# Kernel tuning notes

Measured on AMD Instinct MI355X. Metric: run time of the kernel, lower is better.

## Reference

```python
import jax, jax.numpy as jnp
import numpy as np

N_TOKENS = 8192
D_MODEL = 2048
TOP_K = 2
N_S1 = N_TOKENS * TOP_K  # expanded (token, expert-slot) rows after top-k routing
N_S2 = 8192              # rows re-gathered for the second (intra-node) stage


def setup_inputs() -> dict:
    key = jax.random.key(0)
    k_x, k_i1, k_i2 = jax.random.split(key, 3)
    x = jax.random.normal(k_x, (N_TOKENS, D_MODEL), dtype=jnp.float32)
    # Expanded indices sorted by expert bin (upstream radix-sort of bin_ids).
    indices_s1 = jnp.sort(jax.random.randint(k_i1, (N_S1,), 0, N_S1, dtype=jnp.int64))
    # Map from s1-expert layout rows into the s2 stage layout.
    s1exp_to_s2_indices = jax.random.randint(k_i2, (N_S2,), 0, N_S1, dtype=jnp.int64)
    return {
        "x": x,
        "indices_s1": indices_s1,
        "s1exp_to_s2_indices": s1exp_to_s2_indices,
        "n_tokens": N_TOKENS,
        "top_k": TOP_K,
    }


def reference(x, indices_s1, s1exp_to_s2_indices, n_tokens, top_k):
    # Stage 1: gather_with_token_drop -- expanded index // top_k recovers the
    # source token row; rows are already ordered by expert bin (bins encode
    # capacity/drops, reflected in the length of indices_s1).
    dx_s1 = jnp.take(x, indices_s1 // top_k, axis=0)          # [N_S1, d]
    # _AllToAllSingle(ep_group): pure data exchange; on a single shard the
    # split-and-exchange with ins_s1/outs_s1 is the identity permutation.
    dx_s1_exp = dx_s1
    # Stage 2: s1_to_s2_gather -- re-gather rows into the intra-node layout
    # ordered by (bin_ids_s2, bins_s2).
    dx_s2 = jnp.take(dx_s1_exp, s1exp_to_s2_indices, axis=0)  # [N_S2, d]
    # _AllToAllSingle(local_group): identity on a single shard.
    dx_s2_exp = dx_s2
    # Final local ordering: s2 (intra-node) rows first, then s1 (global) rows.
    return jnp.concatenate([dx_s2_exp, dx_s1_exp], axis=0)    # [N_S2 + N_S1, d]
```

## Files before the change

kernel.cpp:

```cpp
#include <hip/hip_runtime.h>
#include <hip/hip_bf16.h>


typedef float v4f __attribute__((ext_vector_type(4)));

__global__ __launch_bounds__(256) void rb_dispatch_kernel(
    const float* __restrict__ x,
    const int* __restrict__ idx_s1,
    const int* __restrict__ idx_s2,
    const int* __restrict__ top_k_ptr,
    float* __restrict__ out,
    int n_s2, int n_rows, int nvec ) {
  const int wave = threadIdx.x >> 6;
  const int lane = threadIdx.x & 63;
  const int row = blockIdx.x * 4 + wave;
  if (row >= n_rows) return;

  const int top_k = *top_k_ptr;

  int src;
  if (row < n_s2) {
    src = idx_s1[idx_s2[row]] / top_k;
  } else {
    src = idx_s1[row - n_s2] / top_k;
  }

  const int d = nvec * 4;
  const v4f* __restrict__ sp = (const v4f*)(x + (size_t)src * (size_t)d);
  v4f* __restrict__ dp = (v4f*)(out + (size_t)row * (size_t)d);

  #pragma unroll 4
  for (int i = lane; i < nvec; i += 64) {
    v4f v = sp[i];
    __builtin_nontemporal_store(v, dp + i);
  }
}

extern "C" void kernel_launch(void* const* d_in, const int* in_sizes, int n_in,
                              void* d_out, int out_size, void* d_ws, size_t ws_size,
                              hipStream_t stream) {
  const float* x      = (const float*)d_in[0];
  const int*   idx_s1 = (const int*)d_in[1];
  const int*   idx_s2 = (const int*)d_in[2];
  const int*   top_k  = (const int*)d_in[4];
  float*       out    = (float*)d_out;

  const int n_s1   = in_sizes[1];
  const int n_s2   = in_sizes[2];
  const int n_rows = n_s1 + n_s2;
  const int d      = out_size / n_rows;
  const int nvec   = d / 4;

  const int rows_per_block = 4;
  const int grid = (n_rows + rows_per_block - 1) / rows_per_block;

  rb_dispatch_kernel<<<grid, 256, 0, stream>>>(
      x, idx_s1, idx_s2, top_k, out, n_s2, n_rows, nvec);
}
```

Measured before the change: 255.7 us.

## Process two rows per wave with XCD-aware block remap and duplicate-source reuse

Each wave now copies two consecutive output rows instead of one, and the block count is halved. Block indices are remapped so that consecutive logical blocks are spread across the 8 XCDs. For d=2048 the kernel uses a fully unrolled 8-vector register copy, and when both rows share a source token it reuses the loaded registers instead of reading x again. Because the s1 indices are sorted and two slots map to one token, adjacent rows often share a source, which could save reads. The remap assumes n_blocks is divisible by 8; otherwise some blocks would be skipped or duplicated.

```diff
diff --git a/kernel.cpp b/kernel.cpp
--- a/kernel.cpp
+++ b/kernel.cpp
@@ -10,29 +10,57 @@
     const int* __restrict__ idx_s2,
     const int* __restrict__ top_k_ptr,
     float* __restrict__ out,
-    int n_s2, int n_rows, int nvec ) {
+    int n_s2, int n_rows, int n_blocks, int nvec ) {
+  const int b = blockIdx.x;
+  const int v = (b & 7) * (n_blocks >> 3) + (b >> 3);
+
   const int wave = threadIdx.x >> 6;
   const int lane = threadIdx.x & 63;
-  const int row = blockIdx.x * 4 + wave;
-  if (row >= n_rows) return;
+  const int r0 = v * 8 + wave * 2;
+  const int r1 = r0 + 1;
+  if (r0 >= n_rows) return;
 
   const int top_k = *top_k_ptr;
 
-  int src;
-  if (row < n_s2) {
-    src = idx_s1[idx_s2[row]] / top_k;
+  int s0, s1;
+  if (r0 < n_s2) s0 = idx_s1[idx_s2[r0]] / top_k;
+  else           s0 = idx_s1[r0 - n_s2] / top_k;
+  if (r1 < n_s2) s1 = idx_s1[idx_s2[r1]] / top_k;
+  else           s1 = idx_s1[r1 - n_s2] / top_k;
+
+  if (nvec == 512) {
+    const v4f* __restrict__ sp0 = (const v4f*)x + (size_t)s0 * 512;
+    v4f* __restrict__ dp0 = (v4f*)out + (size_t)r0 * 512;
+    v4f* __restrict__ dp1 = (v4f*)out + (size_t)r1 * 512;
+
+    v4f r[8];
+    #pragma unroll
+    for (int k = 0; k < 8; ++k) r[k] = sp0[lane + 64 * k];
+    #pragma unroll
+    for (int k = 0; k < 8; ++k)
+      __builtin_nontemporal_store(r[k], dp0 + lane + 64 * k);
+
+    if (s1 == s0) {
+      #pragma unroll
+      for (int k = 0; k < 8; ++k)
+        __builtin_nontemporal_store(r[k], dp1 + lane + 64 * k);
+    } else {
+      const v4f* __restrict__ sp1 = (const v4f*)x + (size_t)s1 * 512;
+      #pragma unroll
+      for (int k = 0; k < 8; ++k) r[k] = sp1[lane + 64 * k];
+      #pragma unroll
+      for (int k = 0; k < 8; ++k)
+        __builtin_nontemporal_store(r[k], dp1 + lane + 64 * k);
+    }
   } else {
-    src = idx_s1[row - n_s2] / top_k;
-  }
-
-  const int d = nvec * 4;
-  const v4f* __restrict__ sp = (const v4f*)(x + (size_t)src * (size_t)d);
-  v4f* __restrict__ dp = (v4f*)(out + (size_t)row * (size_t)d);
-
-  #pragma unroll 4
-  for (int i = lane; i < nvec; i += 64) {
-    v4f v = sp[i];
-    __builtin_nontemporal_store(v, dp + i);
+    const v4f* sp0 = (const v4f*)x + (size_t)s0 * nvec;
+    const v4f* sp1 = (const v4f*)x + (size_t)s1 * nvec;
+    v4f* dp0 = (v4f*)out + (size_t)r0 * nvec;
+    v4f* dp1 = (v4f*)out + (size_t)r1 * nvec;
+    for (int i = lane; i < nvec; i += 64) {
+      __builtin_nontemporal_store(sp0[i], dp0 + i);
+      __builtin_nontemporal_store(sp1[i], dp1 + i);
+    }
   }
 }
 
@@ -51,9 +79,8 @@
   const int d      = out_size / n_rows;
   const int nvec   = d / 4;
 
-  const int rows_per_block = 4;
-  const int grid = (n_rows + rows_per_block - 1) / rows_per_block;
+  const int n_blocks = (n_rows + 7) / 8;
 
-  rb_dispatch_kernel<<<grid, 256, 0, stream>>>(
-      x, idx_s1, idx_s2, top_k, out, n_s2, n_rows, nvec);
+  rb_dispatch_kernel<<<n_blocks, 256, 0, stream>>>(
+      x, idx_s1, idx_s2, top_k, out, n_s2, n_rows, n_blocks, nvec);
 }
```

Measured after the change: 256.1 us. About the same (+0.2%).
